# Optimization experiments

Measured on AMD Instinct MI355X. Metric: run time of the kernel, lower is better.

Reference implementation:

```python
import jax, jax.numpy as jnp
import numpy as np

N, E = 10000, 640000
IN, HID, OUT = 128, 128, 64


def setup_inputs() -> dict:
    key = jax.random.key(0)
    ks = jax.random.split(key, 4)
    return {
        "x": jax.random.normal(ks[0], (N, IN), jnp.float32),
        "W1": jax.random.normal(ks[1], (IN, HID), jnp.float32) / np.sqrt(IN),
        "b1": jnp.zeros((HID,), jnp.float32),
        "W2": jax.random.normal(ks[2], (HID, OUT), jnp.float32) / np.sqrt(HID),
        "b2": jnp.zeros((OUT,), jnp.float32),
        "edge_index": jax.random.randint(ks[3], (2, E), 0, N, jnp.int32),
    }


def _gcn_conv(x, W, b, src, dst, n_nodes):
    # PyG GCNConv: linear transform, then symmetric-normalized scatter-add.
    h = x @ W                                                        # [N, F_out]
    deg = jax.ops.segment_sum(jnp.ones_like(dst, dtype=h.dtype), dst,
                              num_segments=n_nodes)                  # in-degree incl. self-loops
    dinv = jnp.where(deg > 0, jax.lax.rsqrt(deg), 0.0)               # deg^{-1/2}
    norm = dinv[src] * dinv[dst]                                     # [E+N]
    msgs = h[src] * norm[:, None]                                    # gather + scale
    out = jax.ops.segment_sum(msgs, dst, num_segments=n_nodes)       # scatter-add
    return out + b


def reference(x, W1, b1, W2, b2, edge_index):
    n_nodes = x.shape[0]
    loops = jnp.arange(n_nodes, dtype=edge_index.dtype)
    src = jnp.concatenate([edge_index[0], loops])   # add self-loops
    dst = jnp.concatenate([edge_index[1], loops])
    h = _gcn_conv(x, W1, b1, src, dst, n_nodes)
    h = jax.nn.relu(h)
    return _gcn_conv(h, W2, b2, src, dst, n_nodes)
```

## Files before the change

kernel.cpp:

```cpp
#include <hip/hip_runtime.h>


static constexpr int IN_F  = 128;
static constexpr int HID_F = 128;
static constexpr int OUT_F = 64;
static constexpr int SLOT  = 128;
static constexpr int OVCAP = 4096;

__global__ void zero_cnt_k(int* __restrict__ cnt, int total) {
  int i = blockIdx.x * blockDim.x + threadIdx.x;
  if (i < total) cnt[i] = 0;
}

__global__ void fill_slot_k(const int* __restrict__ src, const int* __restrict__ dst,
                            int* __restrict__ cnt, int* __restrict__ slots,
                            int* __restrict__ ovf_cnt, int2* __restrict__ ovf, int E) {
  int e = blockIdx.x * blockDim.x + threadIdx.x;
  if (e < E) {
    int s = src[e], d = dst[e];
    int pos = atomicAdd(&cnt[d], 1);
    if (pos < SLOT) {
      slots[(long)d * SLOT + pos] = s;
    } else {
      int op = atomicAdd(ovf_cnt, 1);
      if (op < OVCAP) ovf[op] = make_int2(s, d);
    }
  }
}

__global__ void dinv_k(const int* __restrict__ cnt, float* __restrict__ dinv, int N) {
  int i = blockIdx.x * blockDim.x + threadIdx.x;
  if (i < N) dinv[i] = 1.0f / sqrtf((float)(cnt[i] + 1));
}

template<int K, int F, int NB, bool RELU_BIAS>
__global__ __launch_bounds__(F) void gemm_scale_k(
    const float* __restrict__ in, const float* __restrict__ W,
    const float* __restrict__ bin, const float* __restrict__ dinv,
    float* __restrict__ hs, int N) {
  __shared__ float xs[NB][K];
  const int f  = threadIdx.x;
  const int n0 = blockIdx.x * NB;

  for (int i = 0; i < NB; ++i) {
    int n = n0 + i;
    for (int k = f; k < K; k += F) {
      float v = (n < N) ? in[(long)n * K + k] : 0.0f;
      if (RELU_BIAS) v = fmaxf(v + bin[k], 0.0f);
      xs[i][k] = v;
    }
  }
  __syncthreads();

  float acc[NB];
#pragma unroll
  for (int i = 0; i < NB; ++i) acc[i] = 0.0f;

  for (int k = 0; k < K; ++k) {
    float w = W[k * F + f];
#pragma unroll
    for (int i = 0; i < NB; ++i) acc[i] = fmaf(xs[i][k], w, acc[i]);
  }

  for (int i = 0; i < NB; ++i) {
    int n = n0 + i;
    if (n < N) hs[(long)n * F + f] = acc[i] * dinv[n];
  }
}

template<int F, bool ADD_BIAS>
__global__ __launch_bounds__(256) void gather_slot_k(
    const int* __restrict__ cnt, const int* __restrict__ slots,
    const float* __restrict__ dinv, const float* __restrict__ hs,
    const float* __restrict__ bias, float* __restrict__ out, int N) {
  const int wid  = (int)((blockIdx.x * blockDim.x + threadIdx.x) >> 6);
  const int lane = threadIdx.x & 63;
  if (wid >= N) return;
  const int deg  = __builtin_amdgcn_readfirstlane(min(cnt[wid], SLOT));
  const long base = (long)wid * SLOT;

  float ax, ay;
  if (F == 128) {
    const float2 v = *reinterpret_cast<const float2*>(hs + (long)wid * 128 + lane * 2);
    ax = v.x; ay = v.y;
  } else {
    ax = hs[(long)wid * 64 + lane]; ay = 0.0f;
  }

  int j = 0;
  for (; j + 8 <= deg; j += 8) {
    if (F == 128) {
      float2 v0, v1, v2, v3, v4, v5, v6, v7;
      {
        const int s0 = slots[base + j + 0], s1 = slots[base + j + 1];
        const int s2 = slots[base + j + 2], s3 = slots[base + j + 3];
        const int s4 = slots[base + j + 4], s5 = slots[base + j + 5];
        const int s6 = slots[base + j + 6], s7 = slots[base + j + 7];
        const long o = lane * 2;
        v0 = *reinterpret_cast<const float2*>(hs + (long)s0 * 128 + o);
        v1 = *reinterpret_cast<const float2*>(hs + (long)s1 * 128 + o);
        v2 = *reinterpret_cast<const float2*>(hs + (long)s2 * 128 + o);
        v3 = *reinterpret_cast<const float2*>(hs + (long)s3 * 128 + o);
        v4 = *reinterpret_cast<const float2*>(hs + (long)s4 * 128 + o);
        v5 = *reinterpret_cast<const float2*>(hs + (long)s5 * 128 + o);
        v6 = *reinterpret_cast<const float2*>(hs + (long)s6 * 128 + o);
        v7 = *reinterpret_cast<const float2*>(hs + (long)s7 * 128 + o);
      }
      ax += ((v0.x + v1.x) + (v2.x + v3.x)) + ((v4.x + v5.x) + (v6.x + v7.x));
      ay += ((v0.y + v1.y) + (v2.y + v3.y)) + ((v4.y + v5.y) + (v6.y + v7.y));
    } else {
      const int s0 = slots[base + j + 0], s1 = slots[base + j + 1];
      const int s2 = slots[base + j + 2], s3 = slots[base + j + 3];
      const int s4 = slots[base + j + 4], s5 = slots[base + j + 5];
      const int s6 = slots[base + j + 6], s7 = slots[base + j + 7];
      const float v0 = hs[(long)s0 * 64 + lane];
      const float v1 = hs[(long)s1 * 64 + lane];
      const float v2 = hs[(long)s2 * 64 + lane];
      const float v3 = hs[(long)s3 * 64 + lane];
      const float v4 = hs[(long)s4 * 64 + lane];
      const float v5 = hs[(long)s5 * 64 + lane];
      const float v6 = hs[(long)s6 * 64 + lane];
      const float v7 = hs[(long)s7 * 64 + lane];
      ax += ((v0 + v1) + (v2 + v3)) + ((v4 + v5) + (v6 + v7));
    }
  }
  for (; j < deg; ++j) {
    const int s = slots[base + j];
    if (F == 128) {
      const float2 v = *reinterpret_cast<const float2*>(hs + (long)s * 128 + lane * 2);
      ax += v.x; ay += v.y;
    } else {
      ax += hs[(long)s * 64 + lane];
    }
  }

  const float di = dinv[wid];
  if (F == 128) {
    float2 r; r.x = ax * di; r.y = ay * di;
    *reinterpret_cast<float2*>(out + (long)wid * 128 + lane * 2) = r;
  } else {
    float v = ax * di;
    if (ADD_BIAS) v += bias[lane];
    out[(long)wid * 64 + lane] = v;
  }
}

template<int F>
__global__ void ovf_fix_k(const int2* __restrict__ ovf, const int* __restrict__ ovf_cnt,
                          const float* __restrict__ dinv, const float* __restrict__ hs,
                          float* __restrict__ target) {
  int m = *ovf_cnt; if (m > OVCAP) m = OVCAP;
  const int f = threadIdx.x;
  for (int i = 0; i < m; ++i) {
    const int s = ovf[i].x, d = ovf[i].y;
    target[(long)d * F + f] += hs[(long)s * F + f] * dinv[d];
  }
}

extern "C" void kernel_launch(void* const* d_in, const int* in_sizes, int n_in,
                              void* d_out, int out_size, void* d_ws, size_t ws_size,
                              hipStream_t stream) {
  const float* x  = (const float*)d_in[0];
  const float* W1 = (const float*)d_in[1];
  const float* b1 = (const float*)d_in[2];
  const float* W2 = (const float*)d_in[3];
  const float* b2 = (const float*)d_in[4];
  const int*   ei = (const int*)d_in[5];

  const int N = in_sizes[0] / IN_F;
  const int E = in_sizes[5] / 2;
  const int* src = ei;
  const int* dst = ei + E;
  float* out = (float*)d_out;

  const int Npad = (N + 256) & ~255;
  int*   cnt     = (int*)d_ws;
  int*   ovf_cnt = cnt + N;
  int2*  ovf     = (int2*)(cnt + Npad);
  int*   slots   = (int*)(ovf + OVCAP);
  float* dinv    = (float*)(slots + (size_t)N * SLOT);
  float* hs1     = dinv + Npad;
  float* agg1    = hs1 + (size_t)N * HID_F;
  float* hs2     = hs1;

  const int B = 256;
  constexpr int NB = 8;

  zero_cnt_k<<<(N + 1 + B - 1) / B, B, 0, stream>>>(cnt, N + 1);
  fill_slot_k<<<(E + B - 1) / B, B, 0, stream>>>(src, dst, cnt, slots, ovf_cnt, ovf, E);
  dinv_k<<<(N + B - 1) / B, B, 0, stream>>>(cnt, dinv, N);

  gemm_scale_k<IN_F, HID_F, NB, false>
      <<<(N + NB - 1) / NB, HID_F, 0, stream>>>(x, W1, nullptr, dinv, hs1, N);
  gather_slot_k<HID_F, false>
      <<<((size_t)N * 64 + B - 1) / B, B, 0, stream>>>(cnt, slots, dinv, hs1,
                                                       nullptr, agg1, N);
  ovf_fix_k<HID_F><<<1, HID_F, 0, stream>>>(ovf, ovf_cnt, dinv, hs1, agg1);

  gemm_scale_k<HID_F, OUT_F, NB, true>
      <<<(N + NB - 1) / NB, OUT_F, 0, stream>>>(agg1, W2, b1, dinv, hs2, N);
  gather_slot_k<OUT_F, true>
      <<<((size_t)N * 64 + B - 1) / B, B, 0, stream>>>(cnt, slots, dinv, hs2,
                                                       b2, out, N);
  ovf_fix_k<OUT_F><<<1, OUT_F, 0, stream>>>(ovf, ovf_cnt, dinv, hs2, out);
}
```

Before: 194.1 us.

## Fold dinv and overflow fixup into GEMM/gather kernels, vectorize edge binning

Drops the separate dinv kernel: the GEMM and gather kernels now compute deg^-1/2 directly from the count array. The two single-block overflow-fixup kernels are removed, and each gather wave instead scans the overflow list for entries that target its own node. The slot-fill kernel now handles four edges per thread using int4 loads. Together these remove three launches and the serial fixup pass, at the cost of an extra rsqrt per use and an overflow scan in every wave.

Result: no change. 190.8 us (-1.7%).

```diff
diff --git a/kernel.cpp b/kernel.cpp
--- a/kernel.cpp
+++ b/kernel.cpp
@@ -12,31 +12,48 @@
   if (i < total) cnt[i] = 0;
 }
 
+__device__ __forceinline__ void push_edge(int s, int d, int* cnt, int* slots,
+                                          int* ovf_cnt, int2* ovf) {
+  int pos = atomicAdd(&cnt[d], 1);
+  if (pos < SLOT) {
+    slots[(long)d * SLOT + pos] = s;
+  } else {
+    int op = atomicAdd(ovf_cnt, 1);
+    if (op < OVCAP) ovf[op] = make_int2(s, d);
+  }
+}
+
 __global__ void fill_slot_k(const int* __restrict__ src, const int* __restrict__ dst,
                             int* __restrict__ cnt, int* __restrict__ slots,
                             int* __restrict__ ovf_cnt, int2* __restrict__ ovf, int E) {
-  int e = blockIdx.x * blockDim.x + threadIdx.x;
-  if (e < E) {
-    int s = src[e], d = dst[e];
-    int pos = atomicAdd(&cnt[d], 1);
-    if (pos < SLOT) {
-      slots[(long)d * SLOT + pos] = s;
-    } else {
-      int op = atomicAdd(ovf_cnt, 1);
-      if (op < OVCAP) ovf[op] = make_int2(s, d);
-    }
-  }
-}
-
-__global__ void dinv_k(const int* __restrict__ cnt, float* __restrict__ dinv, int N) {
-  int i = blockIdx.x * blockDim.x + threadIdx.x;
-  if (i < N) dinv[i] = 1.0f / sqrtf((float)(cnt[i] + 1));
+  const int t  = blockIdx.x * blockDim.x + threadIdx.x;
+  const int e0 = t * 4;
+  if (e0 >= E) return;
+  if (((E & 3) == 0) && (e0 + 4 <= E)) {
+    const int4 s4 = *reinterpret_cast<const int4*>(src + e0);
+    const int4 d4 = *reinterpret_cast<const int4*>(dst + e0);
+    const int p0 = atomicAdd(&cnt[d4.x], 1);
+    const int p1 = atomicAdd(&cnt[d4.y], 1);
+    const int p2 = atomicAdd(&cnt[d4.z], 1);
+    const int p3 = atomicAdd(&cnt[d4.w], 1);
+    if (p0 < SLOT) slots[(long)d4.x * SLOT + p0] = s4.x;
+    else { int op = atomicAdd(ovf_cnt, 1); if (op < OVCAP) ovf[op] = make_int2(s4.x, d4.x); }
+    if (p1 < SLOT) slots[(long)d4.y * SLOT + p1] = s4.y;
+    else { int op = atomicAdd(ovf_cnt, 1); if (op < OVCAP) ovf[op] = make_int2(s4.y, d4.y); }
+    if (p2 < SLOT) slots[(long)d4.z * SLOT + p2] = s4.z;
+    else { int op = atomicAdd(ovf_cnt, 1); if (op < OVCAP) ovf[op] = make_int2(s4.z, d4.z); }
+    if (p3 < SLOT) slots[(long)d4.w * SLOT + p3] = s4.w;
+    else { int op = atomicAdd(ovf_cnt, 1); if (op < OVCAP) ovf[op] = make_int2(s4.w, d4.w); }
+  } else {
+    const int e1 = min(e0 + 4, E);
+    for (int e = e0; e < e1; ++e) push_edge(src[e], dst[e], cnt, slots, ovf_cnt, ovf);
+  }
 }
 
 template<int K, int F, int NB, bool RELU_BIAS>
 __global__ __launch_bounds__(F) void gemm_scale_k(
     const float* __restrict__ in, const float* __restrict__ W,
-    const float* __restrict__ bin, const float* __restrict__ dinv,
+    const float* __restrict__ bin, const int* __restrict__ cnt,
     float* __restrict__ hs, int N) {
   __shared__ float xs[NB][K];
   const int f  = threadIdx.x;
@@ -64,19 +81,24 @@
 
   for (int i = 0; i < NB; ++i) {
     int n = n0 + i;
-    if (n < N) hs[(long)n * F + f] = acc[i] * dinv[n];
+    if (n < N) {
+      const float di = 1.0f / sqrtf((float)(cnt[n] + 1));
+      hs[(long)n * F + f] = acc[i] * di;
+    }
   }
 }
 
 template<int F, bool ADD_BIAS>
 __global__ __launch_bounds__(256) void gather_slot_k(
     const int* __restrict__ cnt, const int* __restrict__ slots,
-    const float* __restrict__ dinv, const float* __restrict__ hs,
-    const float* __restrict__ bias, float* __restrict__ out, int N) {
+    const int* __restrict__ ovf_cnt, const int2* __restrict__ ovf,
+    const float* __restrict__ hs, const float* __restrict__ bias,
+    float* __restrict__ out, int N) {
   const int wid  = (int)((blockIdx.x * blockDim.x + threadIdx.x) >> 6);
   const int lane = threadIdx.x & 63;
   if (wid >= N) return;
-  const int deg  = __builtin_amdgcn_readfirstlane(min(cnt[wid], SLOT));
+  const int craw = __builtin_amdgcn_readfirstlane(cnt[wid]);
+  const int deg  = min(craw, SLOT);
   const long base = (long)wid * SLOT;
 
   float ax, ay;
@@ -134,7 +156,23 @@
     }
   }
 
-  const float di = dinv[wid];
+  {
+    int m = __builtin_amdgcn_readfirstlane(*ovf_cnt);
+    m = min(m, OVCAP);
+    for (int i = 0; i < m; ++i) {
+      const int2 p = ovf[i];
+      if (p.y == wid) {
+        if (F == 128) {
+          const float2 v = *reinterpret_cast<const float2*>(hs + (long)p.x * 128 + lane * 2);
+          ax += v.x; ay += v.y;
+        } else {
+          ax += hs[(long)p.x * 64 + lane];
+        }
+      }
+    }
+  }
+
+  const float di = 1.0f / sqrtf((float)(craw + 1));
   if (F == 128) {
     float2 r; r.x = ax * di; r.y = ay * di;
     *reinterpret_cast<float2*>(out + (long)wid * 128 + lane * 2) = r;
@@ -142,18 +180,6 @@
     float v = ax * di;
     if (ADD_BIAS) v += bias[lane];
     out[(long)wid * 64 + lane] = v;
-  }
-}
-
-template<int F>
-__global__ void ovf_fix_k(const int2* __restrict__ ovf, const int* __restrict__ ovf_cnt,
-                          const float* __restrict__ dinv, const float* __restrict__ hs,
-                          float* __restrict__ target) {
-  int m = *ovf_cnt; if (m > OVCAP) m = OVCAP;
-  const int f = threadIdx.x;
-  for (int i = 0; i < m; ++i) {
-    const int s = ovf[i].x, d = ovf[i].y;
-    target[(long)d * F + f] += hs[(long)s * F + f] * dinv[d];
   }
 }
 
@@ -178,8 +204,7 @@
   int*   ovf_cnt = cnt + N;
   int2*  ovf     = (int2*)(cnt + Npad);
   int*   slots   = (int*)(ovf + OVCAP);
-  float* dinv    = (float*)(slots + (size_t)N * SLOT);
-  float* hs1     = dinv + Npad;
+  float* hs1     = (float*)(slots + (size_t)N * SLOT);
   float* agg1    = hs1 + (size_t)N * HID_F;
   float* hs2     = hs1;
 
@@ -187,20 +212,18 @@
   constexpr int NB = 8;
 
   zero_cnt_k<<<(N + 1 + B - 1) / B, B, 0, stream>>>(cnt, N + 1);
-  fill_slot_k<<<(E + B - 1) / B, B, 0, stream>>>(src, dst, cnt, slots, ovf_cnt, ovf, E);
-  dinv_k<<<(N + B - 1) / B, B, 0, stream>>>(cnt, dinv, N);
+  fill_slot_k<<<((E + 3) / 4 + B - 1) / B, B, 0, stream>>>(src, dst, cnt, slots,
+                                                           ovf_cnt, ovf, E);
 
   gemm_scale_k<IN_F, HID_F, NB, false>
-      <<<(N + NB - 1) / NB, HID_F, 0, stream>>>(x, W1, nullptr, dinv, hs1, N);
+      <<<(N + NB - 1) / NB, HID_F, 0, stream>>>(x, W1, nullptr, cnt, hs1, N);
   gather_slot_k<HID_F, false>
-      <<<((size_t)N * 64 + B - 1) / B, B, 0, stream>>>(cnt, slots, dinv, hs1,
-                                                       nullptr, agg1, N);
-  ovf_fix_k<HID_F><<<1, HID_F, 0, stream>>>(ovf, ovf_cnt, dinv, hs1, agg1);
+      <<<((size_t)N * 64 + B - 1) / B, B, 0, stream>>>(cnt, slots, ovf_cnt, ovf,
+                                                       hs1, nullptr, agg1, N);
 
   gemm_scale_k<HID_F, OUT_F, NB, true>
-      <<<(N + NB - 1) / NB, OUT_F, 0, stream>>>(agg1, W2, b1, dinv, hs2, N);
+      <<<(N + NB - 1) / NB, OUT_F, 0, stream>>>(agg1, W2, b1, cnt, hs2, N);
   gather_slot_k<OUT_F, true>
-      <<<((size_t)N * 64 + B - 1) / B, B, 0, stream>>>(cnt, slots, dinv, hs2,
-                                                       b2, out, N);
-  ovf_fix_k<OUT_F><<<1, OUT_F, 0, stream>>>(ovf, ovf_cnt, dinv, hs2, out);
-}
+      <<<((size_t)N * 64 + B - 1) / B, B, 0, stream>>>(cnt, slots, ovf_cnt, ovf,
+                                                       hs2, b2, out, N);
+}
```
